# Kernel tuning notes

Hardware: AMD Instinct MI355X
Metric: run time of the kernel (lower is better)

Reference implementation:

```python
import jax, jax.numpy as jnp
import numpy as np

B, T, I, H, O = 128, 1024, 128, 1024, 128

def setup_inputs() -> dict:
    key = jax.random.key(0)
    ks = jax.random.split(key, 11)
    s = 1.0 / np.sqrt(H)  # torch default LSTM init scale
    return {
        "x": jax.random.normal(ks[0], (B, T, I), jnp.float32),
        "sequence_length": jax.random.randint(ks[1], (B,), 0, T, jnp.int64 if jax.config.jax_enable_x64 else jnp.int32),
        "hn": jax.random.normal(ks[2], (B, H), jnp.float32),
        "cn": jax.random.normal(ks[3], (B, H), jnp.float32),
        "output_t": jax.random.normal(ks[4], (B, O), jnp.float32),
        "W_ih": jax.random.normal(ks[5], (4 * H, I + O), jnp.float32) * s,
        "W_hh": jax.random.normal(ks[6], (4 * H, H), jnp.float32) * s,
        "b_ih": jax.random.normal(ks[7], (4 * H,), jnp.float32) * s,
        "b_hh": jax.random.normal(ks[8], (4 * H,), jnp.float32) * s,
        "W_out": jax.random.normal(ks[9], (O, H), jnp.float32) * s,
        "b_out": jax.random.normal(ks[10], (O,), jnp.float32) * s,
    }

def reference(x, sequence_length, hn, cn, output_t, W_ih, W_hh, b_ih, b_hh, W_out, b_out):
    # eval mode (self.training=False): no dropout applied
    Tn = x.shape[1]
    Hd = hn.shape[-1]
    # masks[t, b] = 1.0 if sequence_length[b] > t
    masks = (jnp.arange(Tn)[:, None] < sequence_length[None, :]).astype(x.dtype)  # [T, B]
    xs = jnp.transpose(x, (1, 0, 2))  # [T, B, I]
    bias = b_ih + b_hh

    def step(carry, inp):
        h, c, out_t = carry
        xt, m = inp                      # xt [B,I], m [B]
        m = m[:, None]                   # [B,1]
        lstm_in = jnp.concatenate([xt * m, out_t], axis=-1)  # [B, I+O]
        gates = lstm_in @ W_ih.T + h @ W_hh.T + bias          # [B, 4H]
        i_g, f_g, g_g, o_g = jnp.split(gates, 4, axis=-1)     # torch gate order i,f,g,o
        i_g = jax.nn.sigmoid(i_g)
        f_g = jax.nn.sigmoid(f_g)
        g_g = jnp.tanh(g_g)
        o_g = jax.nn.sigmoid(o_g)
        c = f_g * c + i_g * g_g
        h = o_g * jnp.tanh(c)
        out_t = h @ W_out.T + b_out      # [B, O]
        return (h, c, out_t), out_t * m

    (_, _, _), ys = jax.lax.scan(step, (hn, cn, output_t), (xs, masks))
    return jnp.transpose(ys, (1, 0, 2))  # [B, T, O]
```

## Files before the change

kernel.cpp:

```cpp
#include <hip/hip_runtime.h>
#include <stdint.h>

#define Tn 1024
#define In 128

typedef __attribute__((ext_vector_type(8))) short short8;
typedef __attribute__((ext_vector_type(4))) float f32x4;
typedef unsigned long long u64;

#define WS_WFRAG  0ull
#define WS_WOUT   (WS_WFRAG + 10485760ull)
#define WS_Z0     (WS_WOUT + 262144ull)
#define WS_HBUF   (WS_Z0 + 32768ull)
#define WS_BIAS   (WS_HBUF + 524288ull)
#define WS_CNT    (WS_BIAS + 16384ull)

__device__ __forceinline__ unsigned short f2bf(float f) {
  unsigned u = __builtin_bit_cast(unsigned, f);
  return (unsigned short)((u + 0x7FFFu + ((u >> 16) & 1u)) >> 16);
}
__device__ __forceinline__ float fast_sig(float v) {
  float e = __builtin_amdgcn_exp2f(-1.44269504089f * v);
  return __builtin_amdgcn_rcpf(1.0f + e);
}
__device__ __forceinline__ float fast_tanh(float v) {
  float a = fabsf(v);
  float e = __builtin_amdgcn_exp2f(-2.88539008178f * a);
  float r = (1.0f - e) * __builtin_amdgcn_rcpf(1.0f + e);
  return copysignf(r, v);
}

__global__ void k_wfrag(const float* __restrict__ Wih, const float* __restrict__ Whh,
                        const float* __restrict__ Wout, char* __restrict__ ws) {
  const int u = blockIdx.x, nt = blockIdx.y, kt = blockIdx.z;
  const int lane = threadIdx.x;
  const int col = lane & 15, quad = lane >> 4;
  const int r = nt * 16 + col;
  const int g = r >> 5, jj = r & 31;
  const int n = g * 1024 + u * 32 + jj;
  float v[8];
  if (kt < 32) {
    const int k = kt * 32 + quad * 8;
    #pragma unroll
    for (int e = 0; e < 8; e++) v[e] = Whh[(size_t)n * 1024 + k + e];
    const float* wo = Wih + (size_t)n * 256 + 128;
    for (int o = 0; o < 128; o++) {
      const float wv = wo[o];
      const float* wr = Wout + (size_t)o * 1024 + k;
      #pragma unroll
      for (int e = 0; e < 8; e++) v[e] = fmaf(wv, wr[e], v[e]);
    }
  } else if (kt < 36) {
    const int k = (kt - 32) * 32 + quad * 8;
    #pragma unroll
    for (int e = 0; e < 8; e++) v[e] = Wih[(size_t)n * 256 + k + e];
  } else {
    const int o = (kt - 36) * 32 + quad * 8;
    #pragma unroll
    for (int e = 0; e < 8; e++) v[e] = Wih[(size_t)n * 256 + 128 + o + e];
  }
  short8 pk;
  #pragma unroll
  for (int e = 0; e < 8; e++) pk[e] = (short)f2bf(v[e]);
  *(short8*)(ws + WS_WFRAG + ((size_t)((u * 8 + nt) * 40 + kt) * 64 + lane) * 16) = pk;
}

__global__ void k_misc(const float* __restrict__ Wout, const float* __restrict__ hn,
                       const float* __restrict__ out_t, const float* __restrict__ bout,
                       const float* __restrict__ bih, const float* __restrict__ bhh,
                       const float* __restrict__ Wih, char* __restrict__ ws) {
  const int blk = blockIdx.x, lane = threadIdx.x;
  const int col = lane & 15, quad = lane >> 4;
  if (blk < 256) {
    const int u = blk >> 5, kt = blk & 31;
    const int o = u * 16 + col, j0 = kt * 32 + quad * 8;
    short8 pk;
    #pragma unroll
    for (int e = 0; e < 8; e++) pk[e] = (short)f2bf(Wout[(size_t)o * 1024 + j0 + e]);
    *(short8*)(ws + WS_WOUT + ((size_t)(u * 32 + kt) * 64 + lane) * 16) = pk;
  } else if (blk < 512) {
    const int t2 = blk - 256;
    const int mm = t2 >> 5, kt = t2 & 31;
    const int b = mm * 16 + col, j0 = kt * 32 + quad * 8;
    short8 pk;
    #pragma unroll
    for (int e = 0; e < 8; e++) pk[e] = (short)f2bf(hn[(size_t)b * 1024 + j0 + e]);
    *(short8*)(ws + WS_HBUF + ((size_t)((8 + mm) * 32 + kt) * 64 + lane) * 16) = pk;
  } else if (blk < 544) {
    const int t2 = blk - 512;
    const int mm = t2 >> 2, kz = t2 & 3;
    const int b = mm * 16 + col;
    const int o0 = kz * 32 + quad * 8;
    float acc[8];
    #pragma unroll
    for (int e = 0; e < 8; e++) acc[e] = out_t[(size_t)b * 128 + o0 + e] - bout[o0 + e];
    for (int j = 0; j < 1024; j += 4) {
      const f32x4 h4 = *(const f32x4*)(hn + (size_t)b * 1024 + j);
      #pragma unroll
      for (int e = 0; e < 8; e++) {
        const f32x4 w4 = *(const f32x4*)(Wout + (size_t)(o0 + e) * 1024 + j);
        acc[e] -= h4[0] * w4[0] + h4[1] * w4[1] + h4[2] * w4[2] + h4[3] * w4[3];
      }
    }
    short8 pk;
    #pragma unroll
    for (int e = 0; e < 8; e++) pk[e] = (short)f2bf(acc[e]);
    *(short8*)(ws + WS_Z0 + ((size_t)(mm * 4 + kz) * 64 + lane) * 16) = pk;
  } else if (blk < 608) {
    const int n = (blk - 544) * 64 + lane;
    float v = bih[n] + bhh[n];
    const float* wo = Wih + (size_t)n * 256 + 128;
    for (int o = 0; o < 128; o++) v = fmaf(wo[o], bout[o], v);
    ((float*)(ws + WS_BIAS))[n] = v;
  } else {
    int* c = (int*)(ws + WS_CNT);
    const int base = ((blk - 608) * 64 + lane) * 16;
    #pragma unroll
    for (int k = 0; k < 16; k++) c[base + k] = 0;
  }
}

__launch_bounds__(512, 2)
__global__ void k_main(const float* __restrict__ x, const int* __restrict__ seq,
                       const float* __restrict__ cn, const float* __restrict__ b_out,
                       float* __restrict__ out, char* __restrict__ ws) {
  __shared__ short8 a_lds[40 * 64];
  __shared__ float  gates_lds[128 * 20];
  __shared__ short8 htile[64];
  __shared__ float  ysred[8 * 16 * 20];
  __shared__ float  bias_lds[128];
  __shared__ int    seq_lds[16];

  const int tid  = threadIdx.x;
  const int lane = tid & 63;
  const int w    = tid >> 6;
  const int wg   = blockIdx.x;
  const int m    = wg & 7, u = wg >> 3;

  const char* wfrag = ws + WS_WFRAG;
  const char* woutf = ws + WS_WOUT;
  char* hbuf  = ws + WS_HBUF;
  const float* bias2 = (const float*)(ws + WS_BIAS);
  int* cnt = (int*)(ws + WS_CNT);

  short8 bfr[40];
  {
    const char* base = wfrag + ((size_t)(u * 8 + w) * 40 * 64) * 16 + (size_t)lane * 16;
    #pragma unroll
    for (int kt = 0; kt < 40; kt++) bfr[kt] = *(const short8*)(base + (size_t)kt * 1024);
  }
  if (tid < 16) seq_lds[tid] = seq[m * 16 + tid];
  if (tid < 128) {
    const int g = tid >> 5, jj = tid & 31;
    bias_lds[tid] = bias2[g * 1024 + u * 32 + jj];
  }
  const int b_loc  = tid & 15;
  const int jj_loc = tid >> 4;
  float c_reg = cn[(size_t)(m * 16 + b_loc) * 1024 + u * 32 + jj_loc];
  __syncthreads();

  #pragma unroll 1
  for (int tt = 0; tt <= Tn; tt++) {
    if (tt < Tn && tid < 256) {
      const int kt4 = tid >> 6, ln = tid & 63;
      const int b = ln & 15, quad = ln >> 4;
      const int i0 = kt4 * 32 + quad * 8;
      const float* xp = x + ((size_t)(m * 16 + b) * Tn + tt) * In + i0;
      const float mk = (tt < seq_lds[b]) ? 1.0f : 0.0f;
      const f32x4 x0 = *(const f32x4*)xp;
      const f32x4 x1 = *(const f32x4*)(xp + 4);
      short8 pk;
      pk[0] = (short)f2bf(x0[0] * mk); pk[1] = (short)f2bf(x0[1] * mk);
      pk[2] = (short)f2bf(x0[2] * mk); pk[3] = (short)f2bf(x0[3] * mk);
      pk[4] = (short)f2bf(x1[0] * mk); pk[5] = (short)f2bf(x1[1] * mk);
      pk[6] = (short)f2bf(x1[2] * mk); pk[7] = (short)f2bf(x1[3] * mk);
      a_lds[(32 + kt4) * 64 + ln] = pk;
    }
    if (tt == 0 && tid < 256) {
      const int kz = tid >> 6, ln = tid & 63;
      a_lds[(36 + kz) * 64 + ln] =
          *(const short8*)(ws + WS_Z0 + ((size_t)(m * 4 + kz) * 64 + ln) * 16);
    }
    if (tt >= 1 && tid == 0) {
      while (__hip_atomic_load(&cnt[(tt - 1) * 8 + m], __ATOMIC_RELAXED,
                               __HIP_MEMORY_SCOPE_SYSTEM) < 32) {}
    }
    __syncthreads();
    {
      const u64* src = (const u64*)(hbuf + (size_t)((((tt + 1) & 1) * 8) + m) * 32768);
      u64 tmp[8];
      #pragma unroll
      for (int s = 0; s < 8; s++)
        tmp[s] = __hip_atomic_load(&src[s * 512 + tid], __ATOMIC_RELAXED,
                                   __HIP_MEMORY_SCOPE_SYSTEM);
      u64* dst = (u64*)a_lds;
      #pragma unroll
      for (int s = 0; s < 8; s++) dst[s * 512 + tid] = tmp[s];
    }
    __syncthreads();

    if (tt < Tn) {
      const float bias_v = bias_lds[w * 16 + (lane & 15)];
      f32x4 acc0 = {bias_v, bias_v, bias_v, bias_v};
      f32x4 acc1 = {0.f, 0.f, 0.f, 0.f};
      #pragma unroll
      for (int kt = 0; kt < 36; kt += 2) {
        const short8 a0 = a_lds[kt * 64 + lane];
        const short8 a1 = a_lds[(kt + 1) * 64 + lane];
        acc0 = __builtin_amdgcn_mfma_f32_16x16x32_bf16(a0, bfr[kt], acc0, 0, 0, 0);
        acc1 = __builtin_amdgcn_mfma_f32_16x16x32_bf16(a1, bfr[kt + 1], acc1, 0, 0, 0);
      }
      if (tt == 0) {
        #pragma unroll
        for (int kt = 36; kt < 40; kt += 2) {
          const short8 a0 = a_lds[kt * 64 + lane];
          const short8 a1 = a_lds[(kt + 1) * 64 + lane];
          acc0 = __builtin_amdgcn_mfma_f32_16x16x32_bf16(a0, bfr[kt], acc0, 0, 0, 0);
          acc1 = __builtin_amdgcn_mfma_f32_16x16x32_bf16(a1, bfr[kt + 1], acc1, 0, 0, 0);
        }
      }
      {
        const int r = w * 16 + (lane & 15);
        const int bq = (lane >> 4) * 4;
        f32x4 s;
        s[0] = acc0[0] + acc1[0]; s[1] = acc0[1] + acc1[1];
        s[2] = acc0[2] + acc1[2]; s[3] = acc0[3] + acc1[3];
        *(f32x4*)&gates_lds[r * 20 + bq] = s;
      }
      __syncthreads();
      {
        const float Gi = gates_lds[(0 * 32 + jj_loc) * 20 + b_loc];
        const float Gf = gates_lds[(1 * 32 + jj_loc) * 20 + b_loc];
        const float Gg = gates_lds[(2 * 32 + jj_loc) * 20 + b_loc];
        const float Go = gates_lds[(3 * 32 + jj_loc) * 20 + b_loc];
        const float ig = fast_sig(Gi), fg = fast_sig(Gf);
        const float gg = fast_tanh(Gg), og = fast_sig(Go);
        c_reg = fg * c_reg + ig * gg;
        const float h = og * fast_tanh(c_reg);
        ((short*)htile)[(b_loc + 16 * (jj_loc >> 3)) * 8 + (jj_loc & 7)] = (short)f2bf(h);
      }
      __syncthreads();
      if (tid < 64) {
        const short8 v = htile[lane];
        u64* dstp = (u64*)(hbuf + (size_t)((tt & 1) * 8 + m) * 32768 +
                           (size_t)u * 1024) + (size_t)lane * 2;
        const u64* pv = (const u64*)&v;
        __hip_atomic_store(&dstp[0], pv[0], __ATOMIC_RELAXED, __HIP_MEMORY_SCOPE_SYSTEM);
        __hip_atomic_store(&dstp[1], pv[1], __ATOMIC_RELAXED, __HIP_MEMORY_SCOPE_SYSTEM);
        asm volatile("s_waitcnt vmcnt(0)" ::: "memory");
        if (tid == 0)
          __hip_atomic_fetch_add(&cnt[tt * 8 + m], 1, __ATOMIC_RELAXED,
                                 __HIP_MEMORY_SCOPE_SYSTEM);
      }
    }

    if (u < 8 && tt >= 1) {
      f32x4 yacc = {0.f, 0.f, 0.f, 0.f};
      const char* wob = woutf + ((size_t)(u * 32 + w * 4) * 64 + lane) * 16;
      #pragma unroll
      for (int i = 0; i < 4; i++) {
        const short8 bf = *(const short8*)(wob + (size_t)i * 1024);
        const short8 af = a_lds[(w * 4 + i) * 64 + lane];
        yacc = __builtin_amdgcn_mfma_f32_16x16x32_bf16(af, bf, yacc, 0, 0, 0);
      }
      {
        const int o = lane & 15, bq = (lane >> 4) * 4;
        *(f32x4*)&ysred[(w * 16 + o) * 20 + bq] = yacc;
      }
      __syncthreads();
      if (tid < 256) {
        const int o = tid & 15, b = tid >> 4;
        float s = 0.f;
        #pragma unroll
        for (int q = 0; q < 8; q++) s += ysred[(q * 16 + o) * 20 + b];
        s += b_out[u * 16 + o];
        const float val = ((tt - 1) < seq_lds[b]) ? s : 0.0f;
        out[((size_t)(m * 16 + b) * Tn + (tt - 1)) * 128 + u * 16 + o] = val;
      }
      __syncthreads();
    }
  }
}

extern "C" void kernel_launch(void* const* d_in, const int* in_sizes, int n_in,
                              void* d_out, int out_size, void* d_ws, size_t ws_size,
                              hipStream_t stream) {
  (void)in_sizes; (void)n_in; (void)out_size; (void)ws_size;
  const float* x    = (const float*)d_in[0];
  const int*   seq  = (const int*)d_in[1];
  const float* hn   = (const float*)d_in[2];
  const float* cn   = (const float*)d_in[3];
  const float* outt = (const float*)d_in[4];
  const float* Wih  = (const float*)d_in[5];
  const float* Whh  = (const float*)d_in[6];
  const float* bih  = (const float*)d_in[7];
  const float* bhh  = (const float*)d_in[8];
  const float* Wout = (const float*)d_in[9];
  const float* bout = (const float*)d_in[10];
  float* out = (float*)d_out;
  char* ws = (char*)d_ws;

  hipLaunchKernelGGL(k_wfrag, dim3(32, 8, 40), dim3(64), 0, stream, Wih, Whh, Wout, ws);
  hipLaunchKernelGGL(k_misc, dim3(616), dim3(64), 0, stream, Wout, hn, outt, bout,
                     bih, bhh, Wih, ws);
  void* args[] = {(void*)&x, (void*)&seq, (void*)&cn, (void*)&bout, (void*)&out, (void*)&ws};
  hipLaunchCooperativeKernel((const void*)k_main, dim3(256), dim3(512), args, 0, stream);
}
```

Before: 3.746 ms.

## Map batch groups to XCDs at runtime so h exchange stays in-XCD L2

At kernel start each workgroup reads its hardware XCC ID, all workgroups exchange IDs through a scratch area in the output buffer, and each derives a batch group m equal to its XCD and a rank u. When the mapping is balanced, the per-step hidden-state exchange uses sc0-only loads and stores that can be served by the XCD-local L2 instead of system-scope atomics, and the step counters are laid out per group. This aims to cut cross-die coherence latency on the serial recurrence, at the cost of an extra startup handshake and reliance on cache-coherence behaviour within an XCD.

```diff
diff --git a/kernel.cpp b/kernel.cpp
--- a/kernel.cpp
+++ b/kernel.cpp
@@ -68,7 +68,8 @@
 __global__ void k_misc(const float* __restrict__ Wout, const float* __restrict__ hn,
                        const float* __restrict__ out_t, const float* __restrict__ bout,
                        const float* __restrict__ bih, const float* __restrict__ bhh,
-                       const float* __restrict__ Wih, char* __restrict__ ws) {
+                       const float* __restrict__ Wih, float* __restrict__ outp,
+                       char* __restrict__ ws) {
   const int blk = blockIdx.x, lane = threadIdx.x;
   const int col = lane & 15, quad = lane >> 4;
   if (blk < 256) {
@@ -112,11 +113,15 @@
     const float* wo = Wih + (size_t)n * 256 + 128;
     for (int o = 0; o < 128; o++) v = fmaf(wo[o], bout[o], v);
     ((float*)(ws + WS_BIAS))[n] = v;
-  } else {
+  } else if (blk < 616) {
     int* c = (int*)(ws + WS_CNT);
     const int base = ((blk - 608) * 64 + lane) * 16;
     #pragma unroll
     for (int k = 0; k < 16; k++) c[base + k] = 0;
+  } else {
+    int* c = (int*)outp;
+    #pragma unroll
+    for (int k = 0; k < 8; k++) c[lane * 8 + k] = 0;
   }
 }
 
@@ -135,13 +140,56 @@
   const int lane = tid & 63;
   const int w    = tid >> 6;
   const int wg   = blockIdx.x;
-  const int m    = wg & 7, u = wg >> 3;
+
+  int* cnt = (int*)(ws + WS_CNT);
+
+  int m_, u_, fast_;
+  {
+    int* ids = (int*)ysred;
+    int* scr = (int*)out;
+    if (tid == 0) {
+      int myxcd;
+      asm volatile("s_getreg_b32 %0, hwreg(HW_REG_XCC_ID)" : "=s"(myxcd));
+      myxcd &= 7;
+      ids[259] = myxcd;
+      __hip_atomic_store(&scr[8 + wg], myxcd, __ATOMIC_RELAXED, __HIP_MEMORY_SCOPE_SYSTEM);
+      __hip_atomic_fetch_add(&scr[0], 1, __ATOMIC_ACQ_REL, __HIP_MEMORY_SCOPE_SYSTEM);
+      while (__hip_atomic_load(&scr[0], __ATOMIC_ACQUIRE, __HIP_MEMORY_SCOPE_SYSTEM) < 256) {}
+    }
+    __syncthreads();
+    if (tid < 256)
+      ids[tid] = __hip_atomic_load(&scr[8 + tid], __ATOMIC_RELAXED,
+                                   __HIP_MEMORY_SCOPE_SYSTEM) & 7;
+    __syncthreads();
+    if (tid == 0) {
+      const int myxcd = ids[259];
+      int cx[8] = {0, 0, 0, 0, 0, 0, 0, 0};
+      int rank = 0;
+      for (int i = 0; i < 256; i++) {
+        const int xi = ids[i];
+        cx[xi]++;
+        if (xi == myxcd && i < wg) rank++;
+      }
+      bool bal = true;
+      for (int k = 0; k < 8; k++) bal = bal && (cx[k] == 32);
+      ids[256] = bal ? myxcd : (wg & 7);
+      ids[257] = bal ? rank : (wg >> 3);
+      ids[258] = bal ? 1 : 0;
+      __hip_atomic_fetch_add(&scr[1], 1, __ATOMIC_ACQ_REL, __HIP_MEMORY_SCOPE_SYSTEM);
+      while (__hip_atomic_load(&scr[1], __ATOMIC_ACQUIRE, __HIP_MEMORY_SCOPE_SYSTEM) < 256) {}
+    }
+    __syncthreads();
+    m_ = ids[256]; u_ = ids[257]; fast_ = ids[258];
+    __syncthreads();
+  }
+  const int  m     = m_;
+  const int  u     = u_;
+  const bool fastp = (fast_ != 0);
 
   const char* wfrag = ws + WS_WFRAG;
   const char* woutf = ws + WS_WOUT;
   char* hbuf  = ws + WS_HBUF;
   const float* bias2 = (const float*)(ws + WS_BIAS);
-  int* cnt = (int*)(ws + WS_CNT);
 
   short8 bfr[40];
   {
@@ -182,20 +230,38 @@
           *(const short8*)(ws + WS_Z0 + ((size_t)(m * 4 + kz) * 64 + ln) * 16);
     }
     if (tt >= 1 && tid == 0) {
-      while (__hip_atomic_load(&cnt[(tt - 1) * 8 + m], __ATOMIC_RELAXED,
+      while (__hip_atomic_load(&cnt[m * 1024 + (tt - 1)], __ATOMIC_RELAXED,
                                __HIP_MEMORY_SCOPE_SYSTEM) < 32) {}
     }
     __syncthreads();
     {
-      const u64* src = (const u64*)(hbuf + (size_t)((((tt + 1) & 1) * 8) + m) * 32768);
-      u64 tmp[8];
-      #pragma unroll
-      for (int s = 0; s < 8; s++)
-        tmp[s] = __hip_atomic_load(&src[s * 512 + tid], __ATOMIC_RELAXED,
-                                   __HIP_MEMORY_SCOPE_SYSTEM);
-      u64* dst = (u64*)a_lds;
-      #pragma unroll
-      for (int s = 0; s < 8; s++) dst[s * 512 + tid] = tmp[s];
+      const char* srcb = hbuf + (size_t)((((tt + 1) & 1) * 8) + m) * 32768;
+      if (fastp && tt >= 1) {
+        const f32x4* sp = (const f32x4*)srcb;
+        f32x4 t0, t1, t2, t3;
+        asm volatile(
+            "global_load_dwordx4 %0, %4, off sc0\n\t"
+            "global_load_dwordx4 %1, %5, off sc0\n\t"
+            "global_load_dwordx4 %2, %6, off sc0\n\t"
+            "global_load_dwordx4 %3, %7, off sc0\n\t"
+            "s_waitcnt vmcnt(0)"
+            : "=&v"(t0), "=&v"(t1), "=&v"(t2), "=&v"(t3)
+            : "v"(sp + tid), "v"(sp + 512 + tid), "v"(sp + 1024 + tid),
+              "v"(sp + 1536 + tid)
+            : "memory");
+        f32x4* dst = (f32x4*)a_lds;
+        dst[tid] = t0; dst[512 + tid] = t1; dst[1024 + tid] = t2; dst[1536 + tid] = t3;
+      } else {
+        const u64* src = (const u64*)srcb;
+        u64 tmp[8];
+        #pragma unroll
+        for (int s = 0; s < 8; s++)
+          tmp[s] = __hip_atomic_load(&src[s * 512 + tid], __ATOMIC_RELAXED,
+                                     __HIP_MEMORY_SCOPE_SYSTEM);
+        u64* dst = (u64*)a_lds;
+        #pragma unroll
+        for (int s = 0; s < 8; s++) dst[s * 512 + tid] = tmp[s];
+      }
     }
     __syncthreads();
 
@@ -242,14 +308,20 @@
       __syncthreads();
       if (tid < 64) {
         const short8 v = htile[lane];
-        u64* dstp = (u64*)(hbuf + (size_t)((tt & 1) * 8 + m) * 32768 +
-                           (size_t)u * 1024) + (size_t)lane * 2;
-        const u64* pv = (const u64*)&v;
-        __hip_atomic_store(&dstp[0], pv[0], __ATOMIC_RELAXED, __HIP_MEMORY_SCOPE_SYSTEM);
-        __hip_atomic_store(&dstp[1], pv[1], __ATOMIC_RELAXED, __HIP_MEMORY_SCOPE_SYSTEM);
+        char* dstb = hbuf + (size_t)((tt & 1) * 8 + m) * 32768 + (size_t)u * 1024 +
+                     (size_t)lane * 16;
+        if (fastp) {
+          asm volatile("global_store_dwordx4 %0, %1, off sc0" :: "v"(dstb), "v"(v)
+                       : "memory");
+        } else {
+          u64* dstp = (u64*)dstb;
+          const u64* pv = (const u64*)&v;
+          __hip_atomic_store(&dstp[0], pv[0], __ATOMIC_RELAXED, __HIP_MEMORY_SCOPE_SYSTEM);
+          __hip_atomic_store(&dstp[1], pv[1], __ATOMIC_RELAXED, __HIP_MEMORY_SCOPE_SYSTEM);
+        }
         asm volatile("s_waitcnt vmcnt(0)" ::: "memory");
         if (tid == 0)
-          __hip_atomic_fetch_add(&cnt[tt * 8 + m], 1, __ATOMIC_RELAXED,
+          __hip_atomic_fetch_add(&cnt[m * 1024 + tt], 1, __ATOMIC_RELAXED,
                                  __HIP_MEMORY_SCOPE_SYSTEM);
       }
     }
@@ -301,8 +373,8 @@
   char* ws = (char*)d_ws;
 
   hipLaunchKernelGGL(k_wfrag, dim3(32, 8, 40), dim3(64), 0, stream, Wih, Whh, Wout, ws);
-  hipLaunchKernelGGL(k_misc, dim3(616), dim3(64), 0, stream, Wout, hn, outt, bout,
-                     bih, bhh, Wih, ws);
+  hipLaunchKernelGGL(k_misc, dim3(617), dim3(64), 0, stream, Wout, hn, outt, bout,
+                     bih, bhh, Wih, out, ws);
   void* args[] = {(void*)&x, (void*)&seq, (void*)&cn, (void*)&bout, (void*)&out, (void*)&ws};
   hipLaunchCooperativeKernel((const void*)k_main, dim3(256), dim3(512), args, 0, stream);
 }
```

Result: faster. 3.207 ms (-14.4%).
